# Optimization experiments

Measured on AMD Instinct MI355X. Metric: run time of the kernel, lower is better.

Reference implementation:

```python
import jax, jax.numpy as jnp
import numpy as np

NEG_INF = -1.0e9


def _gru_cell(x, h, W_ih, W_hh, b_ih, b_hh):
    # torch GRU gate order: reset, update, new
    gi = x @ W_ih.T + b_ih          # [B, 3H]
    gh = h @ W_hh.T + b_hh          # [B, 3H]
    i_r, i_z, i_n = jnp.split(gi, 3, axis=-1)
    h_r, h_z, h_n = jnp.split(gh, 3, axis=-1)
    r = jax.nn.sigmoid(i_r + h_r)
    z = jax.nn.sigmoid(i_z + h_z)
    ng = jnp.tanh(i_n + r * h_n)
    return (1.0 - z) * ng + z * h


def setup_inputs() -> dict:
    key = jax.random.key(0)
    n, H, B = 512, 512, 256
    ks = jax.random.split(key, 10)
    s_ih0 = 1.0 / np.sqrt(n)
    s = 1.0 / np.sqrt(H)
    return {
        "batch_size": B,
        "W_ih0": jax.random.normal(ks[0], (3 * H, n), jnp.float32) * s_ih0,
        "W_hh0": jax.random.normal(ks[1], (3 * H, H), jnp.float32) * s,
        "b_ih0": jax.random.normal(ks[2], (3 * H,), jnp.float32) * s,
        "b_hh0": jax.random.normal(ks[3], (3 * H,), jnp.float32) * s,
        "W_ih1": jax.random.normal(ks[4], (3 * H, H), jnp.float32) * s,
        "W_hh1": jax.random.normal(ks[5], (3 * H, H), jnp.float32) * s,
        "b_ih1": jax.random.normal(ks[6], (3 * H,), jnp.float32) * s,
        "b_hh1": jax.random.normal(ks[7], (3 * H,), jnp.float32) * s,
        "W_out": jax.random.normal(ks[8], (n, H), jnp.float32) * s,
        "b_out": jax.random.normal(ks[9], (n,), jnp.float32) * s,
    }


def reference(batch_size, W_ih0, W_hh0, b_ih0, b_hh0,
              W_ih1, W_hh1, b_ih1, b_hh1, W_out, b_out):
    n = W_out.shape[0]
    H = W_out.shape[1]
    B = batch_size

    h0 = jnp.zeros((B, H), jnp.float32)
    h1 = jnp.zeros((B, H), jnp.float32)
    available = jnp.ones((B, n), jnp.bool_)
    inp = jnp.ones((B, n), jnp.float32)
    log_probs = jnp.zeros((B,), jnp.float32)

    step_keys = jax.random.split(jax.random.key(42), n)

    def step(carry, key):
        h0, h1, available, inp, lp = carry
        h0n = _gru_cell(inp, h0, W_ih0, W_hh0, b_ih0, b_hh0)
        h1n = _gru_cell(h0n, h1, W_ih1, W_hh1, b_ih1, b_hh1)
        logits = h1n @ W_out.T + b_out                       # [B, n]
        logits = jnp.where(available, logits, NEG_INF)
        probs = jax.nn.softmax(logits, axis=-1)
        idx = jax.random.categorical(key, logits, axis=-1)   # ~ multinomial(probs)
        p_sel = jnp.take_along_axis(probs, idx[:, None], axis=1)[:, 0]
        lp = lp + jnp.log(p_sel + 1e-9)
        oh = jax.nn.one_hot(idx, n, dtype=jnp.float32)       # row of perm matrix
        available = available & ~jax.nn.one_hot(idx, n, dtype=jnp.bool_)
        return (h0n, h1n, available, oh, lp), oh

    (h0, h1, available, inp, log_probs), rows = jax.lax.scan(
        step, (h0, h1, available, inp, log_probs), step_keys)
    perm_matrix = jnp.transpose(rows, (1, 0, 2))             # [B, n, n]
    return perm_matrix, log_probs
```

## Files before the change

### kernel.cpp

```cpp
#include <hip/hip_runtime.h>
#include <cstdint>
#include <cstddef>

#define BB 256
#define NN 512
#define HH 512
#define G3 1536

typedef short bf16x8 __attribute__((ext_vector_type(8)));
typedef float f32x4 __attribute__((ext_vector_type(4)));

__device__ __align__(16) short g_Whh0[2 * 786432];
__device__ __align__(16) short g_Whh1[2 * 786432];
__device__ __align__(16) short g_Wih1[2 * 786432];
__device__ __align__(16) short g_Wout[2 * 262144];
__device__ __align__(16) short g_h0p[2][2 * 131072];
__device__ __align__(16) short g_h1p[2][2 * 131072];
__device__ __align__(16) float g_h0f[BB * HH];
__device__ __align__(16) float g_h1f[BB * HH];
__device__ __align__(16) float g_gh1[BB * G3];
__device__ __align__(16) float g_logits[2][BB * NN];
__device__ __align__(16) float g_gum[2][BB * NN];
__device__ __align__(16) float g_WihT[NN * G3];
__device__ __align__(16) float g_ones[G3];
__device__ float g_lp[BB];
__device__ unsigned g_avail[2][BB * 16];
__device__ int g_idx[BB];

__device__ __forceinline__ unsigned short bf16_rne(float f) {
  uint32_t u = __float_as_uint(f);
  uint32_t r = u + 0x7FFFu + ((u >> 16) & 1u);
  return (unsigned short)(r >> 16);
}
__device__ __forceinline__ float bf16_to_f(unsigned short h) {
  return __uint_as_float(((uint32_t)h) << 16);
}
__device__ __forceinline__ float sigf(float x) {
  return 1.0f / (1.0f + expf(-x));
}
__device__ __forceinline__ f32x4 mfma16(bf16x8 a, bf16x8 b, f32x4 c) {
  return __builtin_amdgcn_mfma_f32_16x16x32_bf16(a, b, c, 0, 0, 0);
}

__device__ __forceinline__ uint32_t rotl32(uint32_t v, int r) {
  return (v << r) | (v >> (32 - r));
}
__device__ __forceinline__ void threefry2x32(uint32_t k0, uint32_t k1,
                                             uint32_t x0, uint32_t x1,
                                             uint32_t& o0, uint32_t& o1) {
  uint32_t k2 = k0 ^ k1 ^ 0x1BD11BDAu;
  x0 += k0; x1 += k1;
  x0 += x1; x1 = rotl32(x1, 13); x1 ^= x0;
  x0 += x1; x1 = rotl32(x1, 15); x1 ^= x0;
  x0 += x1; x1 = rotl32(x1, 26); x1 ^= x0;
  x0 += x1; x1 = rotl32(x1, 6);  x1 ^= x0;
  x0 += k1; x1 += k2 + 1u;
  x0 += x1; x1 = rotl32(x1, 17); x1 ^= x0;
  x0 += x1; x1 = rotl32(x1, 29); x1 ^= x0;
  x0 += x1; x1 = rotl32(x1, 16); x1 ^= x0;
  x0 += x1; x1 = rotl32(x1, 24); x1 ^= x0;
  x0 += k2; x1 += k0 + 2u;
  x0 += x1; x1 = rotl32(x1, 13); x1 ^= x0;
  x0 += x1; x1 = rotl32(x1, 15); x1 ^= x0;
  x0 += x1; x1 = rotl32(x1, 26); x1 ^= x0;
  x0 += x1; x1 = rotl32(x1, 6);  x1 ^= x0;
  x0 += k0; x1 += k1 + 3u;
  x0 += x1; x1 = rotl32(x1, 17); x1 ^= x0;
  x0 += x1; x1 = rotl32(x1, 29); x1 ^= x0;
  x0 += x1; x1 = rotl32(x1, 16); x1 ^= x0;
  x0 += x1; x1 = rotl32(x1, 24); x1 ^= x0;
  x0 += k1; x1 += k2 + 4u;
  x0 += x1; x1 = rotl32(x1, 13); x1 ^= x0;
  x0 += x1; x1 = rotl32(x1, 15); x1 ^= x0;
  x0 += x1; x1 = rotl32(x1, 26); x1 ^= x0;
  x0 += x1; x1 = rotl32(x1, 6);  x1 ^= x0;
  x0 += k2; x1 += k0 + 5u;
  o0 = x0; o1 = x1;
}

__device__ __forceinline__ float gumbel_from_bits(uint32_t bits) {
  float u = __uint_as_float((bits >> 9) | 0x3f800000u) - 1.0f;
  if (u == 0.0f) u = 1.17549435e-38f;
  return -logf(-logf(u));
}

__global__ __launch_bounds__(256) void init_state_kernel() {
  int i = blockIdx.x * 256 + threadIdx.x;
  if (i < BB * HH) { g_h0f[i] = 0.0f; g_h1f[i] = 0.0f; }
  if (i < 262144) {
    ((uint32_t*)g_h0p)[i] = 0u;
    ((uint32_t*)g_h1p)[i] = 0u;
  }
  if (i < 2 * BB * 16) ((unsigned*)g_avail)[i] = 0xFFFFFFFFu;
  if (i < BB) { g_lp[i] = 0.0f; g_idx[i] = 0; }
}

__global__ __launch_bounds__(256) void ones_row_kernel(
    const float* __restrict__ W_ih0, const float* __restrict__ b_ih0) {
  int j = blockIdx.x * 256 + threadIdx.x;
  if (j < G3) {
    const float* row = W_ih0 + (size_t)j * NN;
    float s = 0.0f;
    for (int k = 0; k < NN; ++k) s += row[k];
    g_ones[j] = s + b_ih0[j];
  }
}

__global__ __launch_bounds__(256) void transpose_kernel(
    const float* __restrict__ in) {
  __shared__ float tile[32][33];
  int bx = blockIdx.x;
  int by = blockIdx.y;
  int tx = threadIdx.x & 31;
  int ty = threadIdx.x >> 5;
  for (int i = 0; i < 32; i += 8)
    tile[ty + i][tx] = in[(size_t)(by * 32 + ty + i) * NN + bx * 32 + tx];
  __syncthreads();
  for (int i = 0; i < 32; i += 8)
    g_WihT[(size_t)(bx * 32 + ty + i) * G3 + by * 32 + tx] = tile[tx][ty + i];
}

__global__ __launch_bounds__(256) void split_kernel(
    const float* __restrict__ W, short* __restrict__ dst, int rows,
    int plane) {
  int i = blockIdx.x * 256 + threadIdx.x;
  if (i >= rows * 64) return;
  int c = i >> 6;
  int jb = i & 63;
  int ci = c & 15;
  int tile = (rows == G3) ? (((c & 511) >> 4) * 3 + (c >> 9)) : (c >> 4);
  int S = jb >> 2, qu = jb & 3;
  int off = (tile * 16 + S) * 512 + qu * 128 + ci * 8;
  const float* src = W + (size_t)c * 512 + jb * 8;
  float v[8];
  *(float4*)v = *(const float4*)src;
  *(float4*)(v + 4) = *(const float4*)(src + 4);
  short hb[8], lb[8];
#pragma unroll
  for (int e = 0; e < 8; ++e) {
    unsigned short h = bf16_rne(v[e]);
    hb[e] = (short)h;
    lb[e] = (short)bf16_rne(v[e] - bf16_to_f(h));
  }
  *(bf16x8*)(dst + off) = *(const bf16x8*)hb;
  *(bf16x8*)(dst + plane + off) = *(const bf16x8*)lb;
}

__global__ __launch_bounds__(256) void k0_sample(
    int t, const float* __restrict__ b_out, float* __restrict__ out_perm,
    float* __restrict__ out_lp) {
  const int mt = blockIdx.x;
  const int tid = threadIdx.x;
  if (t < NN) {
    float* lz = g_logits[t & 1] + mt * 16 * NN;
    for (int i = tid; i < 16 * NN; i += 256) lz[i] = 0.0f;
  }
  if (t == 0) return;
  const int tp = t - 1;
  const int rr = tid >> 4, l16 = tid & 15;
  const int b = mt * 16 + rr;
  const float* lrow = g_logits[tp & 1] + b * NN;
  const float* grow = g_gum[tp & 1] + b * NN;
  unsigned aw = g_avail[tp & 1][b * 16 + l16];

  float best = -1.0f / 0.0f;
  int bi = 0;
  float sum = 0.0f;
  for (int k = 0; k < 32; ++k) {
    int c = l16 * 32 + k;
    float l = lrow[c] + b_out[c];
    bool av = (aw >> k) & 1u;
    float ml = av ? l : -1.0e9f;
    float v = grow[c] + ml;
    if (v > best || (v == best && c < bi)) { best = v; bi = c; }
    sum += av ? expf(l) : 0.0f;
  }
  __shared__ float sv[256];
  __shared__ int si[256];
  __shared__ float ss[256];
  sv[tid] = best; si[tid] = bi; ss[tid] = sum;
  __syncthreads();
  for (int s = 8; s > 0; s >>= 1) {
    if (l16 < s) {
      float v2 = sv[tid + s]; int i2 = si[tid + s];
      if (v2 > sv[tid] || (v2 == sv[tid] && i2 < si[tid])) {
        sv[tid] = v2; si[tid] = i2;
      }
      ss[tid] += ss[tid + s];
    }
    __syncthreads();
  }
  const int sel = si[rr * 16];
  const float ssum = ss[rr * 16];
  unsigned nw = aw;
  if ((sel >> 5) == l16) nw &= ~(1u << (sel & 31));
  g_avail[t & 1][b * 16 + l16] = nw;
  if (l16 == 0) {
    float lsel = lrow[sel] + b_out[sel];
    float p = expf(lsel) / ssum;
    float lpn = g_lp[b] + logf(p + 1e-9f);
    g_lp[b] = lpn;
    out_lp[b] = lpn;
    g_idx[b] = sel;
    out_perm[(size_t)b * NN * NN + (size_t)tp * NN + sel] = 1.0f;
  }
}

__global__ __launch_bounds__(256) void k1_layer0(
    int t, const float* __restrict__ b_ih0, const float* __restrict__ b_hh0,
    const float* __restrict__ b_hh1, const float* __restrict__ b_out,
    float* __restrict__ out_perm, float* __restrict__ out_lp) {
  const int bid = blockIdx.x;
  const int mt = bid >> 4, nb = bid & 15;
  const int tid = threadIdx.x;

  {
    float* lz = g_logits[t & 1];
    const int e0 = tid, e1 = tid + 256;
    lz[(mt * 16 + (e0 >> 5)) * NN + nb * 32 + (e0 & 31)] = 0.0f;
    lz[(mt * 16 + (e1 >> 5)) * NN + nb * 32 + (e1 & 31)] = 0.0f;
  }

  __shared__ float sv[256];
  __shared__ int si[256];
  __shared__ float ss[256];
  __shared__ int sel16[16];

  if (t > 0 && nb < 8) {
    const int tp = t - 1;
    const int rr = tid >> 4, l16 = tid & 15;
    const int b = mt * 16 + rr;
    const float* lrow = g_logits[tp & 1] + b * NN;
    const float* grow = g_gum[tp & 1] + b * NN;
    unsigned aw = g_avail[tp & 1][b * 16 + l16];

    float best = -1.0f / 0.0f;
    int bi = 0;
    float sum = 0.0f;
    for (int k = 0; k < 32; ++k) {
      int c = l16 * 32 + k;
      float l = lrow[c] + b_out[c];
      bool av = (aw >> k) & 1u;
      float ml = av ? l : -1.0e9f;
      float v = grow[c] + ml;
      if (v > best || (v == best && c < bi)) { best = v; bi = c; }
      sum += av ? expf(l) : 0.0f;
    }
    sv[tid] = best; si[tid] = bi; ss[tid] = sum;
    __syncthreads();
    for (int s = 8; s > 0; s >>= 1) {
      if (l16 < s) {
        float v2 = sv[tid + s]; int i2 = si[tid + s];
        if (v2 > sv[tid] || (v2 == sv[tid] && i2 < si[tid])) {
          sv[tid] = v2; si[tid] = i2;
        }
        ss[tid] += ss[tid + s];
      }
      __syncthreads();
    }
    const int sel = si[rr * 16];
    if (l16 == 0) sel16[rr] = sel;
    if (nb == 0) {
      unsigned nw = aw;
      if ((sel >> 5) == l16) nw &= ~(1u << (sel & 31));
      g_avail[t & 1][b * 16 + l16] = nw;
      if (l16 == 0) {
        const float ssum = ss[rr * 16];
        float lsel = lrow[sel] + b_out[sel];
        float p = expf(lsel) / ssum;
        float lpn = g_lp[b] + logf(p + 1e-9f);
        g_lp[b] = lpn;
        out_lp[b] = lpn;
        out_perm[(size_t)b * NN * NN + (size_t)tp * NN + sel] = 1.0f;
      }
    }
    __syncthreads();
  }

  const int w = tid >> 6, ln = tid & 63;
  const int ci = ln & 15, qu = ln >> 4;
  const int lnoff = ln * 8;
  const int rb = t & 1, wb = rb ^ 1;

  f32x4 z = (f32x4){0.f, 0.f, 0.f, 0.f};
  f32x4 acc[3] = {z, z, z};

  const int u = (nb & 7) * 4 + w;
  const short* Ap = (nb < 8) ? g_h0p[rb] : g_h1p[rb];
  const short* Wp = (nb < 8) ? g_Whh0 : g_Whh1;

#pragma unroll
  for (int S = 0; S < 16; ++S) {
    const int aoff = mt * 8192 + S * 512 + lnoff;
    bf16x8 ah = *(const bf16x8*)(Ap + aoff);
    bf16x8 al = *(const bf16x8*)(Ap + 131072 + aoff);
#pragma unroll
    for (int g = 0; g < 3; ++g) {
      const short* wp = Wp + ((u * 3 + g) * 16 + S) * 512 + lnoff;
      bf16x8 bh = *(const bf16x8*)wp;
      bf16x8 bl = *(const bf16x8*)(wp + 786432);
      acc[g] = mfma16(ah, bh, acc[g]);
      acc[g] = mfma16(ah, bl, acc[g]);
      acc[g] = mfma16(al, bh, acc[g]);
    }
  }

  const int h = u * 16 + ci;
  if (nb < 8) {
    const float br = b_hh0[h], bz = b_hh0[HH + h], bn = b_hh0[2 * HH + h];
    const float bi0 = b_ih0[h], bi1 = b_ih0[HH + h], bi2 = b_ih0[2 * HH + h];
#pragma unroll
    for (int r = 0; r < 4; ++r) {
      const int b = mt * 16 + qu * 4 + r;
      float ir, iz, in_;
      if (t == 0) {
        ir = g_ones[h]; iz = g_ones[HH + h]; in_ = g_ones[2 * HH + h];
      } else {
        const float* wr_ = g_WihT + (size_t)sel16[qu * 4 + r] * G3;
        ir = wr_[h] + bi0;
        iz = wr_[HH + h] + bi1;
        in_ = wr_[2 * HH + h] + bi2;
      }
      float rr_ = sigf(ir + acc[0][r] + br);
      float zz = sigf(iz + acc[1][r] + bz);
      float ng = tanhf(in_ + rr_ * (acc[2][r] + bn));
      const int o = b * HH + h;
      float hn = (1.f - zz) * ng + zz * g_h0f[o];
      g_h0f[o] = hn;
      const int off = (b >> 4) * 8192 + (h >> 5) * 512 + ((h >> 3) & 3) * 128 +
                      (b & 15) * 8 + (h & 7);
      unsigned short hi = bf16_rne(hn);
      g_h0p[wb][off] = (short)hi;
      g_h0p[wb][131072 + off] = (short)bf16_rne(hn - bf16_to_f(hi));
    }
  } else {
    const float c0 = b_hh1[h], c1 = b_hh1[HH + h], c2 = b_hh1[2 * HH + h];
#pragma unroll
    for (int r = 0; r < 4; ++r) {
      const int b = mt * 16 + qu * 4 + r;
      float* base = g_gh1 + (size_t)b * G3;
      base[h] = acc[0][r] + c0;
      base[512 + h] = acc[1][r] + c1;
      base[1024 + h] = acc[2][r] + c2;
    }
  }
}

__global__ __launch_bounds__(256) void k2_layer1(
    int t, const float* __restrict__ b_ih1) {
  const int bid = blockIdx.x;
  const int mt = bid >> 3, nb = bid & 7;
  const int tid = threadIdx.x;
  const int w = tid >> 6, ln = tid & 63;
  const int ci = ln & 15, qu = ln >> 4;
  const int lnoff = ln * 8;
  const int wb = (t & 1) ^ 1;

  f32x4 z = (f32x4){0.f, 0.f, 0.f, 0.f};
  f32x4 acc[3] = {z, z, z};
  const int u = nb * 4 + w;

#pragma unroll
  for (int S = 0; S < 16; ++S) {
    const int aoff = mt * 8192 + S * 512 + lnoff;
    bf16x8 ah = *(const bf16x8*)(g_h0p[wb] + aoff);
    bf16x8 al = *(const bf16x8*)(g_h0p[wb] + 131072 + aoff);
#pragma unroll
    for (int g = 0; g < 3; ++g) {
      const short* wp = g_Wih1 + ((u * 3 + g) * 16 + S) * 512 + lnoff;
      bf16x8 bh = *(const bf16x8*)wp;
      bf16x8 bl = *(const bf16x8*)(wp + 786432);
      acc[g] = mfma16(ah, bh, acc[g]);
      acc[g] = mfma16(ah, bl, acc[g]);
      acc[g] = mfma16(al, bh, acc[g]);
    }
  }

  const int h = u * 16 + ci;
  const float bi0 = b_ih1[h], bi1 = b_ih1[HH + h], bi2 = b_ih1[2 * HH + h];
  float hn[4];
#pragma unroll
  for (int r = 0; r < 4; ++r) {
    const int b = mt * 16 + qu * 4 + r;
    const float* base = g_gh1 + (size_t)b * G3;
    float rr_ = sigf(acc[0][r] + bi0 + base[h]);
    float zz = sigf(acc[1][r] + bi1 + base[512 + h]);
    float ng = tanhf(acc[2][r] + bi2 + rr_ * base[1024 + h]);
    const int o = b * HH + h;
    float v = (1.f - zz) * ng + zz * g_h1f[o];
    g_h1f[o] = v;
    hn[r] = v;
    const int off = (b >> 4) * 8192 + (h >> 5) * 512 + ((h >> 3) & 3) * 128 +
                    (b & 15) * 8 + (h & 7);
    unsigned short hi = bf16_rne(v);
    g_h1p[wb][off] = (short)hi;
    g_h1p[wb][131072 + off] = (short)bf16_rne(v - bf16_to_f(hi));
  }

  __shared__ short Lh[1024], Ll[1024];
  const int kk = w * 16 + ci;
#pragma unroll
  for (int r = 0; r < 4; ++r) {
    const int m = qu * 4 + r;
    const int off = (kk >> 5) * 512 + ((kk >> 3) & 3) * 128 + m * 8 + (kk & 7);
    unsigned short hi = bf16_rne(hn[r]);
    Lh[off] = (short)hi;
    Ll[off] = (short)bf16_rne(hn[r] - bf16_to_f(hi));
  }
  __syncthreads();

  f32x4 acc2[8] = {z, z, z, z, z, z, z, z};
#pragma unroll
  for (int S2 = 0; S2 < 2; ++S2) {
    bf16x8 ah = *(const bf16x8*)&Lh[S2 * 512 + lnoff];
    bf16x8 al = *(const bf16x8*)&Ll[S2 * 512 + lnoff];
#pragma unroll
    for (int j = 0; j < 8; ++j) {
      const int nt = w * 8 + j;
      const short* wp = g_Wout + (nt * 16 + nb * 2 + S2) * 512 + lnoff;
      bf16x8 bh = *(const bf16x8*)wp;
      bf16x8 bl = *(const bf16x8*)(wp + 262144);
      acc2[j] = mfma16(ah, bh, acc2[j]);
      acc2[j] = mfma16(ah, bl, acc2[j]);
      acc2[j] = mfma16(al, bh, acc2[j]);
    }
  }
  float* Ldst = g_logits[t & 1];
#pragma unroll
  for (int j = 0; j < 8; ++j) {
    const int n = (w * 8 + j) * 16 + ci;
#pragma unroll
    for (int r = 0; r < 4; ++r) {
      const int b = mt * 16 + qu * 4 + r;
      atomicAdd(&Ldst[b * NN + n], acc2[j][r]);
    }
  }

  if (mt < 8) {
    uint32_t tp_ = (uint32_t)(t & 255);
    uint32_t a0, a1, c0, c1;
    threefry2x32(0u, 42u, 2u * tp_, 2u * tp_ + 512u, a0, a1);
    threefry2x32(0u, 42u, 2u * tp_ + 1u, 2u * tp_ + 1u + 512u, c0, c1);
    uint32_t sk0 = (t < 256) ? a0 : a1;
    uint32_t sk1 = (t < 256) ? c0 : c1;
    float* G = g_gum[t & 1];
    for (int e = tid; e < 1024; e += 256) {
      const int r16 = e >> 6;
      const int c = nb * 64 + (e & 63);
      const int b = mt * 16 + r16;
      uint32_t cnt = (uint32_t)b * 512u + (uint32_t)c;
      uint32_t r0, r1;
      threefry2x32(sk0, sk1, cnt, cnt + 65536u, r0, r1);
      G[b * NN + c] = gumbel_from_bits(r0);
      G[(b + 128) * NN + c] = gumbel_from_bits(r1);
    }
  }
}

extern "C" void kernel_launch(void* const* d_in, const int* in_sizes, int n_in,
                              void* d_out, int out_size, void* d_ws,
                              size_t ws_size, hipStream_t stream) {
  (void)in_sizes; (void)n_in; (void)d_ws; (void)ws_size;
  const float* W_ih0 = (const float*)d_in[1];
  const float* W_hh0 = (const float*)d_in[2];
  const float* b_ih0 = (const float*)d_in[3];
  const float* b_hh0 = (const float*)d_in[4];
  const float* W_ih1 = (const float*)d_in[5];
  const float* W_hh1 = (const float*)d_in[6];
  const float* b_ih1 = (const float*)d_in[7];
  const float* b_hh1 = (const float*)d_in[8];
  const float* W_out = (const float*)d_in[9];
  const float* b_out = (const float*)d_in[10];

  float* out = (float*)d_out;
  float* out_lp = out + (size_t)BB * NN * NN;

  hipMemsetAsync(d_out, 0, (size_t)out_size * sizeof(float), stream);
  init_state_kernel<<<1024, 256, 0, stream>>>();
  ones_row_kernel<<<6, 256, 0, stream>>>(W_ih0, b_ih0);
  transpose_kernel<<<dim3(16, 48), 256, 0, stream>>>(W_ih0);

  short* whh0; hipGetSymbolAddress((void**)&whh0, HIP_SYMBOL(g_Whh0));
  short* whh1; hipGetSymbolAddress((void**)&whh1, HIP_SYMBOL(g_Whh1));
  short* wih1; hipGetSymbolAddress((void**)&wih1, HIP_SYMBOL(g_Wih1));
  short* wout; hipGetSymbolAddress((void**)&wout, HIP_SYMBOL(g_Wout));
  split_kernel<<<384, 256, 0, stream>>>(W_hh0, whh0, G3, 786432);
  split_kernel<<<384, 256, 0, stream>>>(W_hh1, whh1, G3, 786432);
  split_kernel<<<384, 256, 0, stream>>>(W_ih1, wih1, G3, 786432);
  split_kernel<<<128, 256, 0, stream>>>(W_out, wout, NN, 262144);

  for (int t = 0; t < NN; ++t) {
    k1_layer0<<<256, 256, 0, stream>>>(t, b_ih0, b_hh0, b_hh1, b_out, out,
                                       out_lp);
    k2_layer1<<<128, 256, 0, stream>>>(t, b_ih1);
  }
  k0_sample<<<16, 256, 0, stream>>>(NN, b_out, out, out_lp);
}
```

Baseline: 27.09 ms.

## Replace logits atomics with per-block partial buffers and move Gumbel noise to layer0

The k-split output projection used to atomicAdd into a shared logits buffer, and that buffer had to be zeroed every step. Each of the 8 k-slices now writes its own partial logits plane with plain stores, and the sampling code sums the 8 partials plus the bias when it reads them. This drops the atomics and the zeroing pass. Gumbel noise generation also moves from the layer1 kernel to the otherwise idle layer0 blocks (nb>=8). The trade-off is 8x more logits memory and 8x more reads in the sampling path, plus a single logits buffer that now depends on kernel ordering for correctness.

```diff
diff --git a/kernel.cpp b/kernel.cpp
--- a/kernel.cpp
+++ b/kernel.cpp
@@ -19,7 +19,7 @@
 __device__ __align__(16) float g_h0f[BB * HH];
 __device__ __align__(16) float g_h1f[BB * HH];
 __device__ __align__(16) float g_gh1[BB * G3];
-__device__ __align__(16) float g_logits[2][BB * NN];
+__device__ __align__(16) float g_logits_p[8 * BB * NN];
 __device__ __align__(16) float g_gum[2][BB * NN];
 __device__ __align__(16) float g_WihT[NN * G3];
 __device__ __align__(16) float g_ones[G3];
@@ -146,29 +146,54 @@
   *(bf16x8*)(dst + plane + off) = *(const bf16x8*)lb;
 }
 
+__device__ __forceinline__ void load_lv(int b, int l16,
+                                        const float* __restrict__ b_out,
+                                        float* lv) {
+  const float4* bo = (const float4*)(b_out + l16 * 32);
+#pragma unroll
+  for (int k4 = 0; k4 < 8; ++k4) *(float4*)(lv + k4 * 4) = bo[k4];
+#pragma unroll
+  for (int p = 0; p < 8; ++p) {
+    const float4* pr =
+        (const float4*)(g_logits_p + ((size_t)p * BB + b) * NN + l16 * 32);
+#pragma unroll
+    for (int k4 = 0; k4 < 8; ++k4) {
+      float4 v = pr[k4];
+      lv[k4 * 4 + 0] += v.x; lv[k4 * 4 + 1] += v.y;
+      lv[k4 * 4 + 2] += v.z; lv[k4 * 4 + 3] += v.w;
+    }
+  }
+}
+
+__device__ __forceinline__ float lsel_sum(int b, int sel,
+                                          const float* __restrict__ b_out) {
+  float ls = b_out[sel];
+#pragma unroll
+  for (int p = 0; p < 8; ++p) ls += g_logits_p[((size_t)p * BB + b) * NN + sel];
+  return ls;
+}
+
 __global__ __launch_bounds__(256) void k0_sample(
     int t, const float* __restrict__ b_out, float* __restrict__ out_perm,
     float* __restrict__ out_lp) {
   const int mt = blockIdx.x;
   const int tid = threadIdx.x;
-  if (t < NN) {
-    float* lz = g_logits[t & 1] + mt * 16 * NN;
-    for (int i = tid; i < 16 * NN; i += 256) lz[i] = 0.0f;
-  }
   if (t == 0) return;
   const int tp = t - 1;
   const int rr = tid >> 4, l16 = tid & 15;
   const int b = mt * 16 + rr;
-  const float* lrow = g_logits[tp & 1] + b * NN;
   const float* grow = g_gum[tp & 1] + b * NN;
   unsigned aw = g_avail[tp & 1][b * 16 + l16];
+
+  float lv[32];
+  load_lv(b, l16, b_out, lv);
 
   float best = -1.0f / 0.0f;
   int bi = 0;
   float sum = 0.0f;
   for (int k = 0; k < 32; ++k) {
     int c = l16 * 32 + k;
-    float l = lrow[c] + b_out[c];
+    float l = lv[k];
     bool av = (aw >> k) & 1u;
     float ml = av ? l : -1.0e9f;
     float v = grow[c] + ml;
@@ -196,7 +221,7 @@
   if ((sel >> 5) == l16) nw &= ~(1u << (sel & 31));
   g_avail[t & 1][b * 16 + l16] = nw;
   if (l16 == 0) {
-    float lsel = lrow[sel] + b_out[sel];
+    float lsel = lsel_sum(b, sel, b_out);
     float p = expf(lsel) / ssum;
     float lpn = g_lp[b] + logf(p + 1e-9f);
     g_lp[b] = lpn;
@@ -214,13 +239,6 @@
   const int mt = bid >> 4, nb = bid & 15;
   const int tid = threadIdx.x;
 
-  {
-    float* lz = g_logits[t & 1];
-    const int e0 = tid, e1 = tid + 256;
-    lz[(mt * 16 + (e0 >> 5)) * NN + nb * 32 + (e0 & 31)] = 0.0f;
-    lz[(mt * 16 + (e1 >> 5)) * NN + nb * 32 + (e1 & 31)] = 0.0f;
-  }
-
   __shared__ float sv[256];
   __shared__ int si[256];
   __shared__ float ss[256];
@@ -230,16 +248,18 @@
     const int tp = t - 1;
     const int rr = tid >> 4, l16 = tid & 15;
     const int b = mt * 16 + rr;
-    const float* lrow = g_logits[tp & 1] + b * NN;
     const float* grow = g_gum[tp & 1] + b * NN;
     unsigned aw = g_avail[tp & 1][b * 16 + l16];
+
+    float lv[32];
+    load_lv(b, l16, b_out, lv);
 
     float best = -1.0f / 0.0f;
     int bi = 0;
     float sum = 0.0f;
     for (int k = 0; k < 32; ++k) {
       int c = l16 * 32 + k;
-      float l = lrow[c] + b_out[c];
+      float l = lv[k];
       bool av = (aw >> k) & 1u;
       float ml = av ? l : -1.0e9f;
       float v = grow[c] + ml;
@@ -266,7 +286,7 @@
       g_avail[t & 1][b * 16 + l16] = nw;
       if (l16 == 0) {
         const float ssum = ss[rr * 16];
-        float lsel = lrow[sel] + b_out[sel];
+        float lsel = lsel_sum(b, sel, b_out);
         float p = expf(lsel) / ssum;
         float lpn = g_lp[b] + logf(p + 1e-9f);
         g_lp[b] = lpn;
@@ -344,6 +364,27 @@
       base[1024 + h] = acc[2][r] + c2;
     }
   }
+
+  if (nb >= 8 && mt < 8) {
+    const int nb2 = nb & 7;
+    uint32_t tp_ = (uint32_t)(t & 255);
+    uint32_t a0, a1, c0, c1;
+    threefry2x32(0u, 42u, 2u * tp_, 2u * tp_ + 512u, a0, a1);
+    threefry2x32(0u, 42u, 2u * tp_ + 1u, 2u * tp_ + 1u + 512u, c0, c1);
+    uint32_t sk0 = (t < 256) ? a0 : a1;
+    uint32_t sk1 = (t < 256) ? c0 : c1;
+    float* G = g_gum[t & 1];
+    for (int e = tid; e < 1024; e += 256) {
+      const int r16 = e >> 6;
+      const int c = nb2 * 64 + (e & 63);
+      const int b = mt * 16 + r16;
+      uint32_t cnt = (uint32_t)b * 512u + (uint32_t)c;
+      uint32_t r0, r1;
+      threefry2x32(sk0, sk1, cnt, cnt + 65536u, r0, r1);
+      G[b * NN + c] = gumbel_from_bits(r0);
+      G[(b + 128) * NN + c] = gumbel_from_bits(r1);
+    }
+  }
 }
 
 __global__ __launch_bounds__(256) void k2_layer1(
@@ -425,34 +466,14 @@
       acc2[j] = mfma16(al, bh, acc2[j]);
     }
   }
-  float* Ldst = g_logits[t & 1];
+  float* Ldst = g_logits_p + (size_t)nb * BB * NN;
 #pragma unroll
   for (int j = 0; j < 8; ++j) {
     const int n = (w * 8 + j) * 16 + ci;
 #pragma unroll
     for (int r = 0; r < 4; ++r) {
       const int b = mt * 16 + qu * 4 + r;
-      atomicAdd(&Ldst[b * NN + n], acc2[j][r]);
-    }
-  }
-
-  if (mt < 8) {
-    uint32_t tp_ = (uint32_t)(t & 255);
-    uint32_t a0, a1, c0, c1;
-    threefry2x32(0u, 42u, 2u * tp_, 2u * tp_ + 512u, a0, a1);
-    threefry2x32(0u, 42u, 2u * tp_ + 1u, 2u * tp_ + 1u + 512u, c0, c1);
-    uint32_t sk0 = (t < 256) ? a0 : a1;
-    uint32_t sk1 = (t < 256) ? c0 : c1;
-    float* G = g_gum[t & 1];
-    for (int e = tid; e < 1024; e += 256) {
-      const int r16 = e >> 6;
-      const int c = nb * 64 + (e & 63);
-      const int b = mt * 16 + r16;
-      uint32_t cnt = (uint32_t)b * 512u + (uint32_t)c;
-      uint32_t r0, r1;
-      threefry2x32(sk0, sk1, cnt, cnt + 65536u, r0, r1);
-      G[b * NN + c] = gumbel_from_bits(r0);
-      G[(b + 128) * NN + c] = gumbel_from_bits(r1);
+      Ldst[b * NN + n] = acc2[j][r];
     }
   }
 }
```

Result: slower. 29.14 ms (+7.6%).

## Fuse per-step layer kernels into one launch with per-tile atomic flag handoff

Applied to the files above, without the earlier changes.

The two per-timestep kernels (layer0/hidden-gate GEMMs and layer1/output projection) become a single kernel. Each block publishes completion of its batch tile through a release atomic counter, and the first 128 blocks spin on an acquire load for their tile before running the layer-1 and logits stage. Gumbel noise generation moves into the former layer-1 hidden-gate blocks, and the redundant logits zeroing in the final sample kernel is dropped. This halves the number of launches per step and replaces a kernel boundary with fine-grained dependencies, at the cost of spin-waiting. The wait is only deadlock-free if all 256 blocks are co-resident.

```diff
diff --git a/kernel.cpp b/kernel.cpp
--- a/kernel.cpp
+++ b/kernel.cpp
@@ -26,6 +26,7 @@
 __device__ float g_lp[BB];
 __device__ unsigned g_avail[2][BB * 16];
 __device__ int g_idx[BB];
+__device__ int g_done[NN][16];
 
 __device__ __forceinline__ unsigned short bf16_rne(float f) {
   uint32_t u = __float_as_uint(f);
@@ -92,6 +93,7 @@
     ((uint32_t*)g_h1p)[i] = 0u;
   }
   if (i < 2 * BB * 16) ((unsigned*)g_avail)[i] = 0xFFFFFFFFu;
+  if (i < NN * 16) ((int*)g_done)[i] = 0;
   if (i < BB) { g_lp[i] = 0.0f; g_idx[i] = 0; }
 }
 
@@ -151,10 +153,6 @@
     float* __restrict__ out_lp) {
   const int mt = blockIdx.x;
   const int tid = threadIdx.x;
-  if (t < NN) {
-    float* lz = g_logits[t & 1] + mt * 16 * NN;
-    for (int i = tid; i < 16 * NN; i += 256) lz[i] = 0.0f;
-  }
   if (t == 0) return;
   const int tp = t - 1;
   const int rr = tid >> 4, l16 = tid & 15;
@@ -206,13 +204,20 @@
   }
 }
 
-__global__ __launch_bounds__(256) void k1_layer0(
+__global__ __launch_bounds__(256) void step_kernel(
     int t, const float* __restrict__ b_ih0, const float* __restrict__ b_hh0,
-    const float* __restrict__ b_hh1, const float* __restrict__ b_out,
-    float* __restrict__ out_perm, float* __restrict__ out_lp) {
+    const float* __restrict__ b_hh1, const float* __restrict__ b_ih1,
+    const float* __restrict__ b_out, float* __restrict__ out_perm,
+    float* __restrict__ out_lp) {
   const int bid = blockIdx.x;
   const int mt = bid >> 4, nb = bid & 15;
   const int tid = threadIdx.x;
+
+  __shared__ float sv[256];
+  __shared__ int si[256];
+  __shared__ float ss[256];
+  __shared__ int sel16[16];
+  __shared__ short Lh[1024], Ll[1024];
 
   {
     float* lz = g_logits[t & 1];
@@ -220,11 +225,6 @@
     lz[(mt * 16 + (e0 >> 5)) * NN + nb * 32 + (e0 & 31)] = 0.0f;
     lz[(mt * 16 + (e1 >> 5)) * NN + nb * 32 + (e1 & 31)] = 0.0f;
   }
-
-  __shared__ float sv[256];
-  __shared__ int si[256];
-  __shared__ float ss[256];
-  __shared__ int sel16[16];
 
   if (t > 0 && nb < 8) {
     const int tp = t - 1;
@@ -277,182 +277,198 @@
     __syncthreads();
   }
 
-  const int w = tid >> 6, ln = tid & 63;
-  const int ci = ln & 15, qu = ln >> 4;
-  const int lnoff = ln * 8;
-  const int rb = t & 1, wb = rb ^ 1;
-
-  f32x4 z = (f32x4){0.f, 0.f, 0.f, 0.f};
-  f32x4 acc[3] = {z, z, z};
-
-  const int u = (nb & 7) * 4 + w;
-  const short* Ap = (nb < 8) ? g_h0p[rb] : g_h1p[rb];
-  const short* Wp = (nb < 8) ? g_Whh0 : g_Whh1;
-
-#pragma unroll
-  for (int S = 0; S < 16; ++S) {
-    const int aoff = mt * 8192 + S * 512 + lnoff;
-    bf16x8 ah = *(const bf16x8*)(Ap + aoff);
-    bf16x8 al = *(const bf16x8*)(Ap + 131072 + aoff);
-#pragma unroll
-    for (int g = 0; g < 3; ++g) {
-      const short* wp = Wp + ((u * 3 + g) * 16 + S) * 512 + lnoff;
-      bf16x8 bh = *(const bf16x8*)wp;
-      bf16x8 bl = *(const bf16x8*)(wp + 786432);
-      acc[g] = mfma16(ah, bh, acc[g]);
-      acc[g] = mfma16(ah, bl, acc[g]);
-      acc[g] = mfma16(al, bh, acc[g]);
-    }
-  }
-
-  const int h = u * 16 + ci;
-  if (nb < 8) {
-    const float br = b_hh0[h], bz = b_hh0[HH + h], bn = b_hh0[2 * HH + h];
-    const float bi0 = b_ih0[h], bi1 = b_ih0[HH + h], bi2 = b_ih0[2 * HH + h];
+  {
+    const int w = tid >> 6, ln = tid & 63;
+    const int ci = ln & 15, qu = ln >> 4;
+    const int lnoff = ln * 8;
+    const int rb = t & 1, wb = rb ^ 1;
+
+    f32x4 z = (f32x4){0.f, 0.f, 0.f, 0.f};
+    f32x4 acc[3] = {z, z, z};
+
+    const int u = (nb & 7) * 4 + w;
+    const short* Ap = (nb < 8) ? g_h0p[rb] : g_h1p[rb];
+    const short* Wp = (nb < 8) ? g_Whh0 : g_Whh1;
+
+#pragma unroll
+    for (int S = 0; S < 16; ++S) {
+      const int aoff = mt * 8192 + S * 512 + lnoff;
+      bf16x8 ah = *(const bf16x8*)(Ap + aoff);
+      bf16x8 al = *(const bf16x8*)(Ap + 131072 + aoff);
+#pragma unroll
+      for (int g = 0; g < 3; ++g) {
+        const short* wp = Wp + ((u * 3 + g) * 16 + S) * 512 + lnoff;
+        bf16x8 bh = *(const bf16x8*)wp;
+        bf16x8 bl = *(const bf16x8*)(wp + 786432);
+        acc[g] = mfma16(ah, bh, acc[g]);
+        acc[g] = mfma16(ah, bl, acc[g]);
+        acc[g] = mfma16(al, bh, acc[g]);
+      }
+    }
+
+    const int h = u * 16 + ci;
+    if (nb < 8) {
+      const float br = b_hh0[h], bz = b_hh0[HH + h], bn = b_hh0[2 * HH + h];
+      const float bi0 = b_ih0[h], bi1 = b_ih0[HH + h], bi2 = b_ih0[2 * HH + h];
+#pragma unroll
+      for (int r = 0; r < 4; ++r) {
+        const int b = mt * 16 + qu * 4 + r;
+        float ir, iz, in_;
+        if (t == 0) {
+          ir = g_ones[h]; iz = g_ones[HH + h]; in_ = g_ones[2 * HH + h];
+        } else {
+          const float* wr_ = g_WihT + (size_t)sel16[qu * 4 + r] * G3;
+          ir = wr_[h] + bi0;
+          iz = wr_[HH + h] + bi1;
+          in_ = wr_[2 * HH + h] + bi2;
+        }
+        float rr_ = sigf(ir + acc[0][r] + br);
+        float zz = sigf(iz + acc[1][r] + bz);
+        float ng = tanhf(in_ + rr_ * (acc[2][r] + bn));
+        const int o = b * HH + h;
+        float hn = (1.f - zz) * ng + zz * g_h0f[o];
+        g_h0f[o] = hn;
+        const int off = (b >> 4) * 8192 + (h >> 5) * 512 + ((h >> 3) & 3) * 128 +
+                        (b & 15) * 8 + (h & 7);
+        unsigned short hi = bf16_rne(hn);
+        g_h0p[wb][off] = (short)hi;
+        g_h0p[wb][131072 + off] = (short)bf16_rne(hn - bf16_to_f(hi));
+      }
+    } else {
+      const float c0 = b_hh1[h], c1 = b_hh1[HH + h], c2 = b_hh1[2 * HH + h];
+#pragma unroll
+      for (int r = 0; r < 4; ++r) {
+        const int b = mt * 16 + qu * 4 + r;
+        float* base = g_gh1 + (size_t)b * G3;
+        base[h] = acc[0][r] + c0;
+        base[512 + h] = acc[1][r] + c1;
+        base[1024 + h] = acc[2][r] + c2;
+      }
+    }
+
+    if (nb >= 8 && mt < 8) {
+      const int nb2 = nb & 7;
+      uint32_t tp_ = (uint32_t)(t & 255);
+      uint32_t a0, a1, c0, c1;
+      threefry2x32(0u, 42u, 2u * tp_, 2u * tp_ + 512u, a0, a1);
+      threefry2x32(0u, 42u, 2u * tp_ + 1u, 2u * tp_ + 1u + 512u, c0, c1);
+      uint32_t sk0 = (t < 256) ? a0 : a1;
+      uint32_t sk1 = (t < 256) ? c0 : c1;
+      float* G = g_gum[t & 1];
+      for (int e = tid; e < 1024; e += 256) {
+        const int r16 = e >> 6;
+        const int c = nb2 * 64 + (e & 63);
+        const int b = mt * 16 + r16;
+        uint32_t cnt = (uint32_t)b * 512u + (uint32_t)c;
+        uint32_t r0, r1;
+        threefry2x32(sk0, sk1, cnt, cnt + 65536u, r0, r1);
+        G[b * NN + c] = gumbel_from_bits(r0);
+        G[(b + 128) * NN + c] = gumbel_from_bits(r1);
+      }
+    }
+  }
+
+  __syncthreads();
+  if (tid == 0) {
+    __threadfence();
+    __hip_atomic_fetch_add(&g_done[t][mt], 1, __ATOMIC_RELEASE,
+                           __HIP_MEMORY_SCOPE_AGENT);
+  }
+
+  if (bid >= 128) return;
+
+  const int mt2 = bid >> 3, nbk = bid & 7;
+  if (tid == 0) {
+    while (__hip_atomic_load(&g_done[t][mt2], __ATOMIC_ACQUIRE,
+                             __HIP_MEMORY_SCOPE_AGENT) < 16) {
+      __builtin_amdgcn_s_sleep(8);
+    }
+  }
+  __syncthreads();
+
+  {
+    const int w = tid >> 6, ln = tid & 63;
+    const int ci = ln & 15, qu = ln >> 4;
+    const int lnoff = ln * 8;
+    const int wb = (t & 1) ^ 1;
+
+    f32x4 z = (f32x4){0.f, 0.f, 0.f, 0.f};
+    f32x4 acc[3] = {z, z, z};
+    const int u = nbk * 4 + w;
+
+#pragma unroll
+    for (int S = 0; S < 16; ++S) {
+      const int aoff = mt2 * 8192 + S * 512 + lnoff;
+      bf16x8 ah = *(const bf16x8*)(g_h0p[wb] + aoff);
+      bf16x8 al = *(const bf16x8*)(g_h0p[wb] + 131072 + aoff);
+#pragma unroll
+      for (int g = 0; g < 3; ++g) {
+        const short* wp = g_Wih1 + ((u * 3 + g) * 16 + S) * 512 + lnoff;
+        bf16x8 bh = *(const bf16x8*)wp;
+        bf16x8 bl = *(const bf16x8*)(wp + 786432);
+        acc[g] = mfma16(ah, bh, acc[g]);
+        acc[g] = mfma16(ah, bl, acc[g]);
+        acc[g] = mfma16(al, bh, acc[g]);
+      }
+    }
+
+    const int h = u * 16 + ci;
+    const float bi0 = b_ih1[h], bi1 = b_ih1[HH + h], bi2 = b_ih1[2 * HH + h];
+    float hn[4];
 #pragma unroll
     for (int r = 0; r < 4; ++r) {
-      const int b = mt * 16 + qu * 4 + r;
-      float ir, iz, in_;
-      if (t == 0) {
-        ir = g_ones[h]; iz = g_ones[HH + h]; in_ = g_ones[2 * HH + h];
-      } else {
-        const float* wr_ = g_WihT + (size_t)sel16[qu * 4 + r] * G3;
-        ir = wr_[h] + bi0;
-        iz = wr_[HH + h] + bi1;
-        in_ = wr_[2 * HH + h] + bi2;
-      }
-      float rr_ = sigf(ir + acc[0][r] + br);
-      float zz = sigf(iz + acc[1][r] + bz);
-      float ng = tanhf(in_ + rr_ * (acc[2][r] + bn));
+      const int b = mt2 * 16 + qu * 4 + r;
+      const float* base = g_gh1 + (size_t)b * G3;
+      float rr_ = sigf(acc[0][r] + bi0 + base[h]);
+      float zz = sigf(acc[1][r] + bi1 + base[512 + h]);
+      float ng = tanhf(acc[2][r] + bi2 + rr_ * base[1024 + h]);
       const int o = b * HH + h;
-      float hn = (1.f - zz) * ng + zz * g_h0f[o];
-      g_h0f[o] = hn;
+      float v = (1.f - zz) * ng + zz * g_h1f[o];
+      g_h1f[o] = v;
+      hn[r] = v;
       const int off = (b >> 4) * 8192 + (h >> 5) * 512 + ((h >> 3) & 3) * 128 +
                       (b & 15) * 8 + (h & 7);
-      unsigned short hi = bf16_rne(hn);
-      g_h0p[wb][off] = (short)hi;
-      g_h0p[wb][131072 + off] = (short)bf16_rne(hn - bf16_to_f(hi));
-    }
-  } else {
-    const float c0 = b_hh1[h], c1 = b_hh1[HH + h], c2 = b_hh1[2 * HH + h];
+      unsigned short hi = bf16_rne(v);
+      g_h1p[wb][off] = (short)hi;
+      g_h1p[wb][131072 + off] = (short)bf16_rne(v - bf16_to_f(hi));
+    }
+
+    const int kk = w * 16 + ci;
 #pragma unroll
     for (int r = 0; r < 4; ++r) {
-      const int b = mt * 16 + qu * 4 + r;
-      float* base = g_gh1 + (size_t)b * G3;
-      base[h] = acc[0][r] + c0;
-      base[512 + h] = acc[1][r] + c1;
-      base[1024 + h] = acc[2][r] + c2;
-    }
-  }
-}
-
-__global__ __launch_bounds__(256) void k2_layer1(
-    int t, const float* __restrict__ b_ih1) {
-  const int bid = blockIdx.x;
-  const int mt = bid >> 3, nb = bid & 7;
-  const int tid = threadIdx.x;
-  const int w = tid >> 6, ln = tid & 63;
-  const int ci = ln & 15, qu = ln >> 4;
-  const int lnoff = ln * 8;
-  const int wb = (t & 1) ^ 1;
-
-  f32x4 z = (f32x4){0.f, 0.f, 0.f, 0.f};
-  f32x4 acc[3] = {z, z, z};
-  const int u = nb * 4 + w;
-
-#pragma unroll
-  for (int S = 0; S < 16; ++S) {
-    const int aoff = mt * 8192 + S * 512 + lnoff;
-    bf16x8 ah = *(const bf16x8*)(g_h0p[wb] + aoff);
-    bf16x8 al = *(const bf16x8*)(g_h0p[wb] + 131072 + aoff);
-#pragma unroll
-    for (int g = 0; g < 3; ++g) {
-      const short* wp = g_Wih1 + ((u * 3 + g) * 16 + S) * 512 + lnoff;
-      bf16x8 bh = *(const bf16x8*)wp;
-      bf16x8 bl = *(const bf16x8*)(wp + 786432);
-      acc[g] = mfma16(ah, bh, acc[g]);
-      acc[g] = mfma16(ah, bl, acc[g]);
-      acc[g] = mfma16(al, bh, acc[g]);
-    }
-  }
-
-  const int h = u * 16 + ci;
-  const float bi0 = b_ih1[h], bi1 = b_ih1[HH + h], bi2 = b_ih1[2 * HH + h];
-  float hn[4];
-#pragma unroll
-  for (int r = 0; r < 4; ++r) {
-    const int b = mt * 16 + qu * 4 + r;
-    const float* base = g_gh1 + (size_t)b * G3;
-    float rr_ = sigf(acc[0][r] + bi0 + base[h]);
-    float zz = sigf(acc[1][r] + bi1 + base[512 + h]);
-    float ng = tanhf(acc[2][r] + bi2 + rr_ * base[1024 + h]);
-    const int o = b * HH + h;
-    float v = (1.f - zz) * ng + zz * g_h1f[o];
-    g_h1f[o] = v;
-    hn[r] = v;
-    const int off = (b >> 4) * 8192 + (h >> 5) * 512 + ((h >> 3) & 3) * 128 +
-                    (b & 15) * 8 + (h & 7);
-    unsigned short hi = bf16_rne(v);
-    g_h1p[wb][off] = (short)hi;
-    g_h1p[wb][131072 + off] = (short)bf16_rne(v - bf16_to_f(hi));
-  }
-
-  __shared__ short Lh[1024], Ll[1024];
-  const int kk = w * 16 + ci;
-#pragma unroll
-  for (int r = 0; r < 4; ++r) {
-    const int m = qu * 4 + r;
-    const int off = (kk >> 5) * 512 + ((kk >> 3) & 3) * 128 + m * 8 + (kk & 7);
-    unsigned short hi = bf16_rne(hn[r]);
-    Lh[off] = (short)hi;
-    Ll[off] = (short)bf16_rne(hn[r] - bf16_to_f(hi));
-  }
-  __syncthreads();
-
-  f32x4 acc2[8] = {z, z, z, z, z, z, z, z};
-#pragma unroll
-  for (int S2 = 0; S2 < 2; ++S2) {
-    bf16x8 ah = *(const bf16x8*)&Lh[S2 * 512 + lnoff];
-    bf16x8 al = *(const bf16x8*)&Ll[S2 * 512 + lnoff];
+      const int m = qu * 4 + r;
+      const int off = (kk >> 5) * 512 + ((kk >> 3) & 3) * 128 + m * 8 + (kk & 7);
+      unsigned short hi = bf16_rne(hn[r]);
+      Lh[off] = (short)hi;
+      Ll[off] = (short)bf16_rne(hn[r] - bf16_to_f(hi));
+    }
+    __syncthreads();
+
+    f32x4 acc2[8] = {z, z, z, z, z, z, z, z};
+#pragma unroll
+    for (int S2 = 0; S2 < 2; ++S2) {
+      bf16x8 ah = *(const bf16x8*)&Lh[S2 * 512 + lnoff];
+      bf16x8 al = *(const bf16x8*)&Ll[S2 * 512 + lnoff];
+#pragma unroll
+      for (int j = 0; j < 8; ++j) {
+        const int nt = w * 8 + j;
+        const short* wp = g_Wout + (nt * 16 + nbk * 2 + S2) * 512 + lnoff;
+        bf16x8 bh = *(const bf16x8*)wp;
+        bf16x8 bl = *(const bf16x8*)(wp + 262144);
+        acc2[j] = mfma16(ah, bh, acc2[j]);
+        acc2[j] = mfma16(ah, bl, acc2[j]);
+        acc2[j] = mfma16(al, bh, acc2[j]);
+      }
+    }
+    float* Ldst = g_logits[t & 1];
 #pragma unroll
     for (int j = 0; j < 8; ++j) {
-      const int nt = w * 8 + j;
-      const short* wp = g_Wout + (nt * 16 + nb * 2 + S2) * 512 + lnoff;
-      bf16x8 bh = *(const bf16x8*)wp;
-      bf16x8 bl = *(const bf16x8*)(wp + 262144);
-      acc2[j] = mfma16(ah, bh, acc2[j]);
-      acc2[j] = mfma16(ah, bl, acc2[j]);
-      acc2[j] = mfma16(al, bh, acc2[j]);
-    }
-  }
-  float* Ldst = g_logits[t & 1];
-#pragma unroll
-  for (int j = 0; j < 8; ++j) {
-    const int n = (w * 8 + j) * 16 + ci;
-#pragma unroll
-    for (int r = 0; r < 4; ++r) {
-      const int b = mt * 16 + qu * 4 + r;
-      atomicAdd(&Ldst[b * NN + n], acc2[j][r]);
-    }
-  }
-
-  if (mt < 8) {
-    uint32_t tp_ = (uint32_t)(t & 255);
-    uint32_t a0, a1, c0, c1;
-    threefry2x32(0u, 42u, 2u * tp_, 2u * tp_ + 512u, a0, a1);
-    threefry2x32(0u, 42u, 2u * tp_ + 1u, 2u * tp_ + 1u + 512u, c0, c1);
-    uint32_t sk0 = (t < 256) ? a0 : a1;
-    uint32_t sk1 = (t < 256) ? c0 : c1;
-    float* G = g_gum[t & 1];
-    for (int e = tid; e < 1024; e += 256) {
-      const int r16 = e >> 6;
-      const int c = nb * 64 + (e & 63);
-      const int b = mt * 16 + r16;
-      uint32_t cnt = (uint32_t)b * 512u + (uint32_t)c;
-      uint32_t r0, r1;
-      threefry2x32(sk0, sk1, cnt, cnt + 65536u, r0, r1);
-      G[b * NN + c] = gumbel_from_bits(r0);
-      G[(b + 128) * NN + c] = gumbel_from_bits(r1);
+      const int n = (w * 8 + j) * 16 + ci;
+#pragma unroll
+      for (int r = 0; r < 4; ++r) {
+        const int b = mt2 * 16 + qu * 4 + r;
+        atomicAdd(&Ldst[b * NN + n], acc2[j][r]);
+      }
     }
   }
 }
@@ -490,9 +506,8 @@
   split_kernel<<<128, 256, 0, stream>>>(W_out, wout, NN, 262144);
 
   for (int t = 0; t < NN; ++t) {
-    k1_layer0<<<256, 256, 0, stream>>>(t, b_ih0, b_hh0, b_hh1, b_out, out,
-                                       out_lp);
-    k2_layer1<<<128, 256, 0, stream>>>(t, b_ih1);
+    step_kernel<<<256, 256, 0, stream>>>(t, b_ih0, b_hh0, b_hh1, b_ih1,
+                                         b_out, out, out_lp);
   }
   k0_sample<<<16, 256, 0, stream>>>(NN, b_out, out, out_lp);
 }
```

After: 40.81 ms. +50.6%, slower.
